# Optimization experiments

Hardware: AMD Instinct MI355X
Metric: run time of the kernel (lower is better)

## Reference

```python
import jax, jax.numpy as jnp
import numpy as np

NEG_INF = -1e30  # stands in for float('-inf') masked_fill; safe under softmax
MAX_ITERS = 6


def setup_inputs() -> dict:
    key = jax.random.key(0)
    ks = jax.random.split(key, 8)
    B, T, D, Dp, E = 8, 1500, 1536, 1024, 192
    s = lambda fan_in: 1.0 / np.sqrt(fan_in)
    return {
        "h": jax.random.normal(ks[0], (B, T, D), jnp.float32),
        "W1": jax.random.normal(ks[1], (3 * D, Dp), jnp.float32) * s(3 * D),
        "Wc": jax.random.normal(ks[2], (D, Dp), jnp.float32) * s(D),
        "W2": jax.random.normal(ks[3], (Dp, D), jnp.float32) * s(Dp),
        "b2": jnp.zeros((D,), jnp.float32),
        "w0": jax.random.normal(ks[4], (2 * D, E), jnp.float32) * s(2 * D),
        "b0": jnp.zeros((E,), jnp.float32),
        "Wstop": jax.random.normal(ks[5], (2 * D, 1), jnp.float32) * s(2 * D),
        "bstop": jnp.zeros((1,), jnp.float32),
        "threshold": jnp.full((1,), 0.5, jnp.float32),
        "C0": jnp.zeros((D,), jnp.float32),
    }


def _weighted_stats(h, a):
    # h: [B,T,D], a broadcastable to [B,T,D]
    mu = jnp.sum(a * h, axis=1)                         # [B,D]
    second = jnp.sum(a * h * h, axis=1)                 # [B,D]
    sigma = jnp.sqrt(jnp.clip(second - mu * mu, 1e-8))
    return mu, sigma


def reference(h, W1, Wc, W2, b2, w0, b0, Wstop, bstop, threshold, C0):
    B, T, D = h.shape
    th = threshold[0]

    # a_init = 1/T is constant across iterations -> hoist uniform stats and W1(e)
    mu0, sigma0 = _weighted_stats(h, jnp.float32(1.0 / T))          # [B,D]
    e = jnp.concatenate(
        [h,
         jnp.broadcast_to(mu0[:, None, :], (B, T, D)),
         jnp.broadcast_to(sigma0[:, None, :], (B, T, D))], axis=-1)  # [B,T,3D]
    base = jnp.einsum('btk,kp->btp', e, W1)                          # [B,T,Dp]

    energy_mask = jnp.mean(h * h, axis=-1) > 1e-4                    # [B,T]

    C = jnp.broadcast_to(C0[None, :], (B, D))
    stop = jnp.zeros((B,), bool)
    mask = jnp.ones((B, MAX_ITERS), bool)
    iters = jnp.arange(MAX_ITERS)

    embs, probs = [], []
    for i in range(MAX_ITERS):
        out1 = base + (C @ Wc)[:, None, :]                           # [B,T,Dp]
        out2 = jax.nn.relu(out1) @ W2 + b2                           # [B,T,D]
        att_raw = jnp.mean(out2, axis=-1)                            # [B,T]
        att_raw = jnp.where(energy_mask, att_raw, NEG_INF)
        A = jax.nn.softmax(att_raw, axis=-1)
        A = A / (jnp.sum(A, axis=1, keepdims=True) + 1e-8)

        # NOTE: faithful to source -- second weighted_stats uses out2 ('a'), not A
        mu_p, sigma_p = _weighted_stats(h, out2)                     # [B,D]
        emb = jnp.concatenate([mu_p, sigma_p], axis=-1) @ w0 + b0    # [B,E]
        emb = emb / jnp.maximum(
            jnp.linalg.norm(emb, axis=-1, keepdims=True), 1e-12)

        active = (~stop).astype(h.dtype)[:, None]
        C = C + active * (jnp.einsum('bt,btd->bd', A, h) / T)

        z = jnp.concatenate([jnp.sum(A[:, :, None] * out2, axis=1), C], axis=-1)
        p = jax.nn.sigmoid(z @ Wstop + bstop)[:, 0]                  # [B]

        newly = p < th
        mask = mask & ~(newly[:, None] & (iters[None, :] >= i))
        stop = stop | newly
        embs.append(emb)
        probs.append(p)

    E = jnp.stack(embs, axis=1)                                      # [B,6,E]
    E = E * mask[:, :, None].astype(E.dtype)
    P = jnp.stack(probs, axis=1)                                     # [B,6]
    return E, P
```

## Files before the change

### kernel.cpp

```cpp
#include <hip/hip_runtime.h>
#include <math.h>

#define NB 8
#define NT 1500
#define ND 1536
#define NP 1024
#define NE 192
#define NITER 6
#define NEGINF -1e30f

typedef __attribute__((ext_vector_type(8))) short bf16x8;
typedef __attribute__((ext_vector_type(4))) float f32x4;
typedef __attribute__((ext_vector_type(8))) unsigned short us16x8;

__device__ __forceinline__ unsigned short bf_rne(float x) {
    unsigned u = __float_as_uint(x);
    return (unsigned short)((u + 0x7FFFu + ((u >> 16) & 1u)) >> 16);
}
__device__ __forceinline__ float bf_f(unsigned short u) {
    return __uint_as_float(((unsigned)u) << 16);
}

__device__ __forceinline__ float block_reduce_sum(float v, float* red) {
    int tid = threadIdx.x;
    red[tid] = v; __syncthreads();
    for (int s = blockDim.x >> 1; s > 0; s >>= 1) {
        if (tid < s) red[tid] += red[tid + s];
        __syncthreads();
    }
    float r = red[0]; __syncthreads();
    return r;
}

__global__ void k_colstats(const float* __restrict__ h, float* __restrict__ sum1,
                           float* __restrict__ sum2) {
    int d = blockIdx.x * 256 + threadIdx.x;
    int b = blockIdx.y;
    int t0 = blockIdx.z * 125, t1 = t0 + 125;
    const float* hp = h + (size_t)b * NT * ND + d;
    float s = 0.f, s2 = 0.f;
    for (int t = t0; t < t1; ++t) { float v = hp[(size_t)t * ND]; s += v; s2 += v * v; }
    atomicAdd(&sum1[b * ND + d], s);
    atomicAdd(&sum2[b * ND + d], s2);
}

__global__ void k_stats_fin(float* __restrict__ mu0, float* __restrict__ sig0) {
    int i = blockIdx.x * 256 + threadIdx.x;
    float mu = mu0[i] * (1.f / NT);
    float sec = sig0[i] * (1.f / NT);
    mu0[i] = mu;
    sig0[i] = sqrtf(fmaxf(sec - mu * mu, 1e-8f));
}

__global__ void k_energy(const float* __restrict__ h, float* __restrict__ emask) {
    __shared__ float red[256];
    int t = blockIdx.x, b = blockIdx.y;
    const float* hp = h + ((size_t)b * NT + t) * ND;
    float s = 0.f;
    for (int d = threadIdx.x; d < ND; d += 256) { float v = hp[d]; s += v * v; }
    s = block_reduce_sum(s, red);
    if (threadIdx.x == 0) emask[b * NT + t] = (s * (1.f / ND) > 1e-4f) ? 1.f : 0.f;
}

__global__ void k_w2r(const float* __restrict__ W2, const float* __restrict__ b2,
                      float* __restrict__ w2r, float* __restrict__ b2m) {
    __shared__ float red[256];
    int p = blockIdx.x;
    float s = 0.f;
    if (p < NP) {
        const float* row = W2 + (size_t)p * ND;
        for (int d = threadIdx.x; d < ND; d += 256) s += row[d];
        s = block_reduce_sum(s, red);
        if (threadIdx.x == 0) w2r[p] = s * (1.f / ND);
    } else {
        for (int d = threadIdx.x; d < ND; d += 256) s += b2[d];
        s = block_reduce_sum(s, red);
        if (threadIdx.x == 0) b2m[0] = s * (1.f / ND);
    }
}

__global__ void k_biasb(const float* __restrict__ W1, const float* __restrict__ mu0,
                        const float* __restrict__ sig0, float* __restrict__ biasb) {
    int p = blockIdx.x * 256 + threadIdx.x;
    int d0 = blockIdx.y * 192, d1 = d0 + 192;
    float acc[NB];
#pragma unroll
    for (int b = 0; b < NB; ++b) acc[b] = 0.f;
    for (int d = d0; d < d1; ++d) {
        float wa = W1[(size_t)(ND + d) * NP + p];
        float wb = W1[(size_t)(2 * ND + d) * NP + p];
#pragma unroll
        for (int b = 0; b < NB; ++b)
            acc[b] += mu0[b * ND + d] * wa + sig0[b * ND + d] * wb;
    }
#pragma unroll
    for (int b = 0; b < NB; ++b) atomicAdd(&biasb[b * NP + p], acc[b]);
}

__global__ void k_init(float* __restrict__ C, const float* __restrict__ C0,
                       float* __restrict__ stopf) {
    int d = blockIdx.x * 256 + threadIdx.x;
    int b = blockIdx.y;
    C[b * ND + d] = C0[d];
    if (blockIdx.x == 0 && threadIdx.x == 0) stopf[b] = 0.f;
}

__global__ void k_split_w(const float* __restrict__ W, int ldw, int kcnt,
                          unsigned short* __restrict__ th, unsigned short* __restrict__ tl) {
    __shared__ float t[128][33];
    int nt = blockIdx.x, kc = blockIdx.y, tid = threadIdx.x;
    int col = tid & 127, kh = tid >> 7;
    const float* wp = W + (size_t)(kc * 32 + kh) * ldw + nt * 128 + col;
#pragma unroll
    for (int i = 0; i < 16; ++i)
        t[col][kh + 2 * i] = wp[(size_t)(2 * i) * ldw];
    __syncthreads();
    int r = tid >> 1;
    int swz = (r >> 1) & 3;
    size_t tb = ((size_t)nt * kcnt + kc) * 4096;
#pragma unroll
    for (int j = 0; j < 2; ++j) {
        int so = (tid & 1) * 2 + j;
        int s = so ^ swz;
        us16x8 hv, lv;
#pragma unroll
        for (int q = 0; q < 8; ++q) {
            float x = t[r][s * 8 + q];
            unsigned short hh = bf_rne(x);
            hv[q] = hh;
            lv[q] = bf_rne(x - bf_f(hh));
        }
        *(us16x8*)&th[tb + r * 32 + so * 8] = hv;
        *(us16x8*)&tl[tb + r * 32 + so * 8] = lv;
    }
}

__global__ void k_relu_att(const float* __restrict__ base, const float* __restrict__ cvec,
                           const float* __restrict__ w2r, unsigned short* __restrict__ th,
                           float* __restrict__ att) {
    int tr = blockIdx.x, kc = blockIdx.y, b = blockIdx.z;
    int tid = threadIdx.x;
    int r = tid >> 1, quad = tid & 1;
    int row = tr * 128 + r;
    bool ok = row < NT;
    size_t tb = ((size_t)(b * 12 + tr) * 32 + kc) * 4096;
    const float* bp = base + ((size_t)b * NT + row) * NP + kc * 32 + quad * 16;
    const float* cv = cvec + b * NP + kc * 32 + quad * 16;
    const float* wr = w2r + kc * 32 + quad * 16;
    int swz = (r >> 1) & 3;
    float asum = 0.f;
#pragma unroll
    for (int half = 0; half < 2; ++half) {
        us16x8 hv;
#pragma unroll
        for (int j = 0; j < 2; ++j) {
            float x0 = 0.f, x1 = 0.f, x2 = 0.f, x3 = 0.f;
            if (ok) {
                float4 v = *(const float4*)(bp + half * 8 + j * 4);
                float4 c4 = *(const float4*)(cv + half * 8 + j * 4);
                float4 w4 = *(const float4*)(wr + half * 8 + j * 4);
                x0 = fmaxf(v.x + c4.x, 0.f); x1 = fmaxf(v.y + c4.y, 0.f);
                x2 = fmaxf(v.z + c4.z, 0.f); x3 = fmaxf(v.w + c4.w, 0.f);
                asum += x0 * w4.x + x1 * w4.y + x2 * w4.z + x3 * w4.w;
            }
            hv[j * 4 + 0] = bf_rne(x0); hv[j * 4 + 1] = bf_rne(x1);
            hv[j * 4 + 2] = bf_rne(x2); hv[j * 4 + 3] = bf_rne(x3);
        }
        int off = r * 32 + (((quad * 2 + half) ^ swz) << 3);
        *(us16x8*)&th[tb + off] = hv;
    }
    asum += __shfl_xor(asum, 1);
    if (ok && quad == 0) atomicAdd(&att[b * NT + row], asum);
}

__global__ __launch_bounds__(256, 4) void k_gemm_relu(
    const float* __restrict__ hsrc, const unsigned short* __restrict__ at_h,
    const unsigned short* __restrict__ bt_h, const float* __restrict__ b2,
    const float* __restrict__ Aw, float* __restrict__ mup, float* __restrict__ s2p,
    float* __restrict__ zab, float* __restrict__ ahb) {
    constexpr int KC = NP / 32;
    __shared__ unsigned short As[2][4096];
    __shared__ unsigned short Bs[2][4096];
    int flat = blockIdx.x + 12 * (blockIdx.y + 12 * blockIdx.z);
    int swzf = (flat & 7) * 144 + (flat >> 3);
    int tr = swzf % 12, nt = (swzf / 12) % 12, b = swzf / 144;
    int tid = threadIdx.x;
    int lane = tid & 63, w = tid >> 6;
    int wr = w >> 1, wc = w & 1;
    int l15 = lane & 15, kg = lane >> 4;
    int sw = (l15 >> 1) & 3;
    f32x4 acc[4][4];
#pragma unroll
    for (int m = 0; m < 4; ++m)
#pragma unroll
        for (int n = 0; n < 4; ++n) acc[m][n] = (f32x4){0.f, 0.f, 0.f, 0.f};
    int aoff[4], boff[4];
#pragma unroll
    for (int m = 0; m < 4; ++m) aoff[m] = (wr * 64 + m * 16 + l15) * 32 + ((kg ^ sw) << 3);
#pragma unroll
    for (int n = 0; n < 4; ++n) boff[n] = (wc * 64 + n * 16 + l15) * 32 + ((kg ^ sw) << 3);

    const unsigned short* ga = at_h + ((size_t)(b * 12 + tr) * KC) * 4096 + lane * 8;
    const unsigned short* gb = bt_h + ((size_t)nt * KC) * 4096 + lane * 8;

    auto stage = [&](int buf, int kc) {
#pragma unroll
        for (int c = 0; c < 4; ++c) {
            int seg = w * 4 + c;
            int part = seg & 7;
            const unsigned short* src = ((seg >> 3) == 0 ? ga : gb) + (size_t)kc * 4096 + part * 512;
            unsigned short* dst = ((seg >> 3) == 0 ? &As[buf][0] : &Bs[buf][0]) + part * 512;
            __builtin_amdgcn_global_load_lds(src, dst, 16, 0, 0);
        }
    };

    stage(0, 0);
    __syncthreads();
    int cur = 0;
    for (int kc = 0; kc < KC; ++kc) {
        if (kc + 1 < KC) stage(cur ^ 1, kc + 1);
        bf16x8 af[4], bf[4];
#pragma unroll
        for (int m = 0; m < 4; ++m) af[m] = *(const bf16x8*)&As[cur][aoff[m]];
#pragma unroll
        for (int n = 0; n < 4; ++n) bf[n] = *(const bf16x8*)&Bs[cur][boff[n]];
#pragma unroll
        for (int n = 0; n < 4; ++n)
#pragma unroll
            for (int m = 0; m < 4; ++m)
                acc[m][n] = __builtin_amdgcn_mfma_f32_16x16x32_bf16(af[m], bf[n], acc[m][n], 0, 0, 0);
        __syncthreads();
        cur ^= 1;
    }

    int rowb = tr * 128 + wr * 64 + (kg << 2);
    int colb = nt * 128 + wc * 64 + l15;
    float b2c[4];
#pragma unroll
    for (int n = 0; n < 4; ++n) b2c[n] = b2[colb + n * 16];
    float pm[4] = {0, 0, 0, 0}, ps2[4] = {0, 0, 0, 0}, pza[4] = {0, 0, 0, 0}, pah[4] = {0, 0, 0, 0};
#pragma unroll
    for (int m = 0; m < 4; ++m) {
#pragma unroll
        for (int q = 0; q < 4; ++q) {
            int row = rowb + m * 16 + q;
            bool ok = row < NT;
            int rowc = ok ? row : (NT - 1);
            float okf = ok ? 1.f : 0.f;
            float a = Aw[b * NT + rowc] * okf;
            const float* hrow = hsrc + ((size_t)b * NT + rowc) * ND;
#pragma unroll
            for (int n = 0; n < 4; ++n) {
                float hv = hrow[colb + n * 16] * okf;
                float o2 = acc[m][n][q] + b2c[n];
                pm[n] = fmaf(o2, hv, pm[n]);
                ps2[n] = fmaf(o2 * hv, hv, ps2[n]);
                pza[n] = fmaf(a, o2, pza[n]);
                pah[n] = fmaf(a, hv, pah[n]);
            }
        }
    }
#pragma unroll
    for (int n = 0; n < 4; ++n) {
        pm[n] += __shfl_xor(pm[n], 16); pm[n] += __shfl_xor(pm[n], 32);
        ps2[n] += __shfl_xor(ps2[n], 16); ps2[n] += __shfl_xor(ps2[n], 32);
        pza[n] += __shfl_xor(pza[n], 16); pza[n] += __shfl_xor(pza[n], 32);
        pah[n] += __shfl_xor(pah[n], 16); pah[n] += __shfl_xor(pah[n], 32);
        if (kg == 0) {
            int col = colb + n * 16;
            atomicAdd(&mup[b * ND + col], pm[n]);
            atomicAdd(&s2p[b * ND + col], ps2[n]);
            atomicAdd(&zab[b * ND + col], pza[n]);
            atomicAdd(&ahb[b * ND + col], pah[n]);
        }
    }
}

__global__ __launch_bounds__(256, 4) void k_gemm_base(
    const float* __restrict__ hsrc, const unsigned short* __restrict__ bt_h,
    const unsigned short* __restrict__ bt_l, const float* __restrict__ biasb,
    float* __restrict__ Out) {
    constexpr int KC = ND / 32;
    __shared__ unsigned short As[4096];
    __shared__ unsigned short Bh_s[4096];
    __shared__ unsigned short Bl_s[4096];
    int flat = blockIdx.x + 12 * (blockIdx.y + 8 * blockIdx.z);
    int swzf = (flat & 7) * 96 + (flat >> 3);
    int tr = swzf % 12, nt = (swzf / 12) % 8, b = swzf / 96;
    int tid = threadIdx.x;
    int lane = tid & 63, w = tid >> 6;
    int wr = w >> 1, wc = w & 1;
    int l15 = lane & 15, kg = lane >> 4;
    int sw = (l15 >> 1) & 3;
    f32x4 acc[4][4];
#pragma unroll
    for (int m = 0; m < 4; ++m)
#pragma unroll
        for (int n = 0; n < 4; ++n) acc[m][n] = (f32x4){0.f, 0.f, 0.f, 0.f};
    int aoff[4], boff[4];
#pragma unroll
    for (int m = 0; m < 4; ++m) aoff[m] = (wr * 64 + m * 16 + l15) * 32 + ((kg ^ sw) << 3);
#pragma unroll
    for (int n = 0; n < 4; ++n) boff[n] = (wc * 64 + n * 16 + l15) * 32 + ((kg ^ sw) << 3);

    const unsigned short* gbh = bt_h + ((size_t)nt * KC) * 4096 + lane * 8;
    const unsigned short* gbl = bt_l + ((size_t)nt * KC) * 4096 + lane * 8;

    int r2 = tid >> 1, quad = tid & 1;
    int arow = tr * 128 + r2;
    bool aok = arow < NT;
    int aswz = (r2 >> 1) & 3;
    const float* hp = hsrc + ((size_t)b * NT + arow) * ND + quad * 16;

    for (int kc = 0; kc < KC; ++kc) {
#pragma unroll
        for (int c = 0; c < 4; ++c) {
            int seg = w * 4 + c;
            int part = seg & 7;
            const unsigned short* src =
                ((seg >> 3) == 0 ? gbh : gbl) + (size_t)kc * 4096 + part * 512;
            unsigned short* dst = ((seg >> 3) == 0 ? &Bh_s[0] : &Bl_s[0]) + part * 512;
            __builtin_amdgcn_global_load_lds(src, dst, 16, 0, 0);
        }
#pragma unroll
        for (int i = 0; i < 4; ++i) {
            int kk = quad * 16 + i * 4;
            float x0 = 0.f, x1 = 0.f, x2 = 0.f, x3 = 0.f;
            if (aok) {
                float4 v = *(const float4*)(hp + kc * 32 + i * 4);
                x0 = v.x; x1 = v.y; x2 = v.z; x3 = v.w;
            }
            int off = r2 * 32 + (((kk >> 3) ^ aswz) << 3) + (kk & 7);
            *(ushort4*)&As[off] = make_ushort4(bf_rne(x0), bf_rne(x1), bf_rne(x2), bf_rne(x3));
        }
        __syncthreads();
        bf16x8 af[4];
#pragma unroll
        for (int m = 0; m < 4; ++m) af[m] = *(const bf16x8*)&As[aoff[m]];
#pragma unroll
        for (int n = 0; n < 4; ++n) {
            bf16x8 bh = *(const bf16x8*)&Bh_s[boff[n]];
            bf16x8 bl = *(const bf16x8*)&Bl_s[boff[n]];
#pragma unroll
            for (int m = 0; m < 4; ++m) {
                acc[m][n] = __builtin_amdgcn_mfma_f32_16x16x32_bf16(af[m], bh, acc[m][n], 0, 0, 0);
                acc[m][n] = __builtin_amdgcn_mfma_f32_16x16x32_bf16(af[m], bl, acc[m][n], 0, 0, 0);
            }
        }
        __syncthreads();
    }

    int rowb = tr * 128 + wr * 64 + (kg << 2);
    int colb = nt * 128 + wc * 64 + l15;
#pragma unroll
    for (int m = 0; m < 4; ++m)
#pragma unroll
        for (int q = 0; q < 4; ++q) {
            int row = rowb + m * 16 + q;
            if (row < NT) {
                float* orow = Out + ((size_t)b * NT + row) * NP;
#pragma unroll
                for (int n = 0; n < 4; ++n)
                    orow[colb + n * 16] = acc[m][n][q] + biasb[b * NP + colb + n * 16];
            }
        }
}

__global__ void k_cvec(const float* __restrict__ C, const float* __restrict__ Wc,
                       float* __restrict__ cvec) {
    int p = blockIdx.x * 256 + threadIdx.x;
    int d0 = blockIdx.y * 48, d1 = d0 + 48;
    float acc[NB];
#pragma unroll
    for (int b = 0; b < NB; ++b) acc[b] = 0.f;
    for (int d = d0; d < d1; ++d) {
        float wc = Wc[(size_t)d * NP + p];
#pragma unroll
        for (int b = 0; b < NB; ++b) acc[b] += C[b * ND + d] * wc;
    }
#pragma unroll
    for (int b = 0; b < NB; ++b) atomicAdd(&cvec[b * NP + p], acc[b]);
}

__global__ void k_softmax(const float* __restrict__ att, const float* __restrict__ emask,
                          const float* __restrict__ b2m, float* __restrict__ A) {
    __shared__ float red[256];
    int b = blockIdx.x, tid = threadIdx.x;
    float bm = b2m[0];
    const float* x = att + (size_t)b * NT;
    const float* em = emask + (size_t)b * NT;
    float* a = A + (size_t)b * NT;
    float mx = -3.4e38f;
    for (int t = tid; t < NT; t += 256) {
        float v = (em[t] > 0.5f) ? x[t] + bm : NEGINF;
        mx = fmaxf(mx, v);
    }
    red[tid] = mx; __syncthreads();
    for (int s = 128; s > 0; s >>= 1) {
        if (tid < s) red[tid] = fmaxf(red[tid], red[tid + s]);
        __syncthreads();
    }
    mx = red[0]; __syncthreads();
    float sm = 0.f;
    for (int t = tid; t < NT; t += 256) {
        float v = (em[t] > 0.5f) ? x[t] + bm : NEGINF;
        float e = expf(v - mx); a[t] = e; sm += e;
    }
    float s1 = block_reduce_sum(sm, red);
    float inv1 = 1.f / s1;
    float sm2 = 0.f;
    for (int t = tid; t < NT; t += 256) { float v = a[t] * inv1; a[t] = v; sm2 += v; }
    float s2 = block_reduce_sum(sm2, red);
    float inv2 = 1.f / (s2 + 1e-8f);
    for (int t = tid; t < NT; t += 256) a[t] *= inv2;
}

__global__ void k_embacc(const float* __restrict__ red4, const float* __restrict__ w0,
                         float* __restrict__ embt) {
    __shared__ float mus[NB][48], sgs[NB][48];
    int e = threadIdx.x;
    int d0 = blockIdx.x * 48;
    const float* mup = red4;
    const float* s2p = red4 + (size_t)NB * ND;
    for (int idx = e; idx < NB * 48; idx += 192) {
        int b = idx / 48, dd = idx % 48;
        float mu = mup[b * ND + d0 + dd];
        mus[b][dd] = mu;
        sgs[b][dd] = sqrtf(fmaxf(s2p[b * ND + d0 + dd] - mu * mu, 1e-8f));
    }
    __syncthreads();
    float acc[NB];
#pragma unroll
    for (int b = 0; b < NB; ++b) acc[b] = 0.f;
    for (int dd = 0; dd < 48; ++dd) {
        float wa = w0[(size_t)(d0 + dd) * NE + e];
        float wb = w0[(size_t)(ND + d0 + dd) * NE + e];
#pragma unroll
        for (int b = 0; b < NB; ++b)
            acc[b] += mus[b][dd] * wa + sgs[b][dd] * wb;
    }
#pragma unroll
    for (int b = 0; b < NB; ++b) atomicAdd(&embt[b * NE + e], acc[b]);
}

__global__ void k_tail2(const float* __restrict__ red4, const float* __restrict__ embt,
                        const float* __restrict__ b0, const float* __restrict__ Wstop,
                        const float* __restrict__ bstop, const float* __restrict__ thr,
                        float* __restrict__ Cb, float* __restrict__ stopf,
                        float* __restrict__ Eout, float* __restrict__ Pout, int iter) {
    __shared__ float red[256];
    __shared__ float liveflag;
    int b = blockIdx.x, tid = threadIdx.x;
    const float* Ahb = red4 + (size_t)2 * NB * ND + b * ND;
    const float* zAb = red4 + (size_t)3 * NB * ND + b * ND;
    float active = (stopf[b] > 0.5f) ? 0.f : 1.f;
    float dsum = 0.f;
    for (int d = tid; d < ND; d += 256) {
        float Cn = Cb[b * ND + d] + active * (Ahb[d] * (1.f / NT));
        Cb[b * ND + d] = Cn;
        dsum += zAb[d] * Wstop[d] + Cn * Wstop[ND + d];
    }
    float s = block_reduce_sum(dsum, red);
    if (tid == 0) {
        float logit = s + bstop[0];
        float p = 1.f / (1.f + expf(-logit));
        Pout[b * NITER + iter] = p;
        bool newly = p < thr[0];
        if (newly) stopf[b] = 1.f;
        liveflag = (active > 0.5f && !newly) ? 1.f : 0.f;
    }
    __syncthreads();
    float live = liveflag;
    float emb = (tid < NE) ? (embt[b * NE + tid] + b0[tid]) : 0.f;
    float nrm = block_reduce_sum(emb * emb, red);
    float sc = live / fmaxf(sqrtf(nrm), 1e-12f);
    if (tid < NE) Eout[((size_t)b * NITER + iter) * NE + tid] = emb * sc;
}

extern "C" void kernel_launch(void* const* d_in, const int* in_sizes, int n_in,
                              void* d_out, int out_size, void* d_ws, size_t ws_size,
                              hipStream_t stream) {
    const float* h = (const float*)d_in[0];
    const float* W1 = (const float*)d_in[1];
    const float* Wc = (const float*)d_in[2];
    const float* W2 = (const float*)d_in[3];
    const float* b2 = (const float*)d_in[4];
    const float* w0 = (const float*)d_in[5];
    const float* b0 = (const float*)d_in[6];
    const float* Wstop = (const float*)d_in[7];
    const float* bstop = (const float*)d_in[8];
    const float* thr = (const float*)d_in[9];
    const float* C0 = (const float*)d_in[10];

    float* Eout = (float*)d_out;
    float* Pout = Eout + (size_t)NB * NITER * NE;

    char* wsb = (char*)d_ws;
    size_t off = 0;
    auto alloc = [&](size_t bytes) -> void* {
        void* p = wsb + off; off += (bytes + 15) & ~(size_t)15; return p;
    };

    float* base = (float*)alloc((size_t)NB * NT * NP * 4);
    unsigned short* rel_h = (unsigned short*)alloc((size_t)NB * 12 * 32 * 4096 * 2);
    unsigned short* w1t_h = (unsigned short*)alloc((size_t)8 * 48 * 4096 * 2);
    unsigned short* w1t_l = (unsigned short*)alloc((size_t)8 * 48 * 4096 * 2);
    unsigned short* w2t_h = (unsigned short*)alloc((size_t)12 * 32 * 4096 * 2);
    unsigned short* w2t_l = (unsigned short*)alloc((size_t)12 * 32 * 4096 * 2);
    float* mu0 = (float*)alloc((size_t)2 * NB * ND * 4);
    float* sig0 = mu0 + NB * ND;
    float* emask = (float*)alloc(NB * NT * 4);
    float* biasb = (float*)alloc(NB * NP * 4);
    float* w2r = (float*)alloc(NP * 4);
    float* b2m = (float*)alloc(16);
    size_t zelems = (size_t)NB * NP + NB * NT + 4 * NB * ND + NB * NE;
    float* cvec = (float*)alloc(zelems * 4);
    float* att = cvec + NB * NP;
    float* red4 = att + NB * NT;
    float* mup = red4;
    float* s2p = red4 + NB * ND;
    float* zAb = red4 + 3 * NB * ND;
    float* Ahb = red4 + 2 * NB * ND;
    float* embt = red4 + 4 * NB * ND;
    float* Abuf = (float*)alloc(NB * NT * 4);
    float* Cb = (float*)alloc(NB * ND * 4);
    float* stopf = (float*)alloc(32);
    size_t zero_bytes = zelems * 4;

    hipMemsetAsync(mu0, 0, (size_t)2 * NB * ND * 4, stream);
    hipMemsetAsync(biasb, 0, (size_t)NB * NP * 4, stream);
    k_colstats<<<dim3(ND / 256, NB, 12), 256, 0, stream>>>(h, mu0, sig0);
    k_stats_fin<<<dim3(NB * ND / 256), 256, 0, stream>>>(mu0, sig0);
    k_energy<<<dim3(NT, NB), 256, 0, stream>>>(h, emask);
    k_w2r<<<dim3(NP + 1), 256, 0, stream>>>(W2, b2, w2r, b2m);
    k_biasb<<<dim3(NP / 256, 8), 256, 0, stream>>>(W1, mu0, sig0, biasb);
    k_split_w<<<dim3(8, 48), 256, 0, stream>>>(W1, NP, 48, w1t_h, w1t_l);
    k_split_w<<<dim3(12, 32), 256, 0, stream>>>(W2, ND, 32, w2t_h, w2t_l);
    k_gemm_base<<<dim3(12, 8, NB), 256, 0, stream>>>(h, w1t_h, w1t_l, biasb, base);
    k_init<<<dim3(ND / 256, NB), 256, 0, stream>>>(Cb, C0, stopf);

    for (int i = 0; i < NITER; ++i) {
        hipMemsetAsync(cvec, 0, zero_bytes, stream);
        k_cvec<<<dim3(4, 32), 256, 0, stream>>>(Cb, Wc, cvec);
        k_relu_att<<<dim3(12, 32, NB), 256, 0, stream>>>(base, cvec, w2r, rel_h, att);
        k_softmax<<<dim3(NB), 256, 0, stream>>>(att, emask, b2m, Abuf);
        k_gemm_relu<<<dim3(12, 12, NB), 256, 0, stream>>>(
            h, rel_h, w2t_h, b2, Abuf, mup, s2p, zAb, Ahb);
        k_embacc<<<dim3(32), 192, 0, stream>>>(red4, w0, embt);
        k_tail2<<<dim3(NB), 256, 0, stream>>>(red4, embt, b0, Wstop, bstop, thr,
                                              Cb, stopf, Eout, Pout, i);
    }
}
```

Baseline: 1.086 ms.

## Pre-split h to bf16 tiles, store base in bf16, fuse energy computation

Adds a kernel that converts h once into swizzled bf16 tiles and accumulates per-row energy, replacing the separate energy kernel. The base GEMM and the per-iteration GEMM epilogue now read bf16 h tiles instead of fp32 h. The base activations are stored as bf16, halving per-iteration reads in relu_att. Both GEMMs stage 64-wide K chunks in one buffer instead of double-buffered 32-wide chunks. The aim is less memory traffic; the cost is lower precision in base and in the h used for the weighted stats, plus less load/compute overlap in the GEMM loops.

After: 1.120 ms. 3.1% more time.

```diff
diff --git a/kernel.cpp b/kernel.cpp
--- a/kernel.cpp
+++ b/kernel.cpp
@@ -50,16 +50,6 @@
     float sec = sig0[i] * (1.f / NT);
     mu0[i] = mu;
     sig0[i] = sqrtf(fmaxf(sec - mu * mu, 1e-8f));
-}
-
-__global__ void k_energy(const float* __restrict__ h, float* __restrict__ emask) {
-    __shared__ float red[256];
-    int t = blockIdx.x, b = blockIdx.y;
-    const float* hp = h + ((size_t)b * NT + t) * ND;
-    float s = 0.f;
-    for (int d = threadIdx.x; d < ND; d += 256) { float v = hp[d]; s += v * v; }
-    s = block_reduce_sum(s, red);
-    if (threadIdx.x == 0) emask[b * NT + t] = (s * (1.f / ND) > 1e-4f) ? 1.f : 0.f;
 }
 
 __global__ void k_w2r(const float* __restrict__ W2, const float* __restrict__ b2,
@@ -135,34 +125,66 @@
     }
 }
 
-__global__ void k_relu_att(const float* __restrict__ base, const float* __restrict__ cvec,
-                           const float* __restrict__ w2r, unsigned short* __restrict__ th,
-                           float* __restrict__ att) {
+__global__ void k_split_h(const float* __restrict__ h, unsigned short* __restrict__ th,
+                          float* __restrict__ energy) {
+    int tr = blockIdx.x, kc = blockIdx.y, b = blockIdx.z;
+    int tid = threadIdx.x;
+    int r = tid >> 1, quad = tid & 1;
+    int row = tr * 128 + r;
+    bool ok = row < NT;
+    size_t tb = ((size_t)(b * 12 + tr) * 48 + kc) * 4096;
+    const float* hp = h + ((size_t)b * NT + (ok ? row : 0)) * ND + kc * 32 + quad * 16;
+    int swz = (r >> 1) & 3;
+    float es = 0.f;
+#pragma unroll
+    for (int half = 0; half < 2; ++half) {
+        us16x8 hv;
+#pragma unroll
+        for (int j = 0; j < 2; ++j) {
+            float x0 = 0.f, x1 = 0.f, x2 = 0.f, x3 = 0.f;
+            if (ok) {
+                float4 v = *(const float4*)(hp + half * 8 + j * 4);
+                x0 = v.x; x1 = v.y; x2 = v.z; x3 = v.w;
+                es += x0 * x0 + x1 * x1 + x2 * x2 + x3 * x3;
+            }
+            hv[j * 4 + 0] = bf_rne(x0); hv[j * 4 + 1] = bf_rne(x1);
+            hv[j * 4 + 2] = bf_rne(x2); hv[j * 4 + 3] = bf_rne(x3);
+        }
+        int off = r * 32 + (((quad * 2 + half) ^ swz) << 3);
+        *(us16x8*)&th[tb + off] = hv;
+    }
+    es += __shfl_xor(es, 1);
+    if (ok && quad == 0) atomicAdd(&energy[b * NT + row], es);
+}
+
+__global__ void k_relu_att(const unsigned short* __restrict__ base16,
+                           const float* __restrict__ cvec, const float* __restrict__ w2r,
+                           unsigned short* __restrict__ th, float* __restrict__ att) {
     int tr = blockIdx.x, kc = blockIdx.y, b = blockIdx.z;
     int tid = threadIdx.x;
     int r = tid >> 1, quad = tid & 1;
     int row = tr * 128 + r;
     bool ok = row < NT;
     size_t tb = ((size_t)(b * 12 + tr) * 32 + kc) * 4096;
-    const float* bp = base + ((size_t)b * NT + row) * NP + kc * 32 + quad * 16;
+    const unsigned short* bp = base16 + ((size_t)b * NT + (ok ? row : 0)) * NP + kc * 32 + quad * 16;
     const float* cv = cvec + b * NP + kc * 32 + quad * 16;
     const float* wr = w2r + kc * 32 + quad * 16;
     int swz = (r >> 1) & 3;
     float asum = 0.f;
 #pragma unroll
     for (int half = 0; half < 2; ++half) {
+        us16x8 bv = (us16x8){0, 0, 0, 0, 0, 0, 0, 0};
+        if (ok) bv = *(const us16x8*)(bp + half * 8);
         us16x8 hv;
 #pragma unroll
         for (int j = 0; j < 2; ++j) {
-            float x0 = 0.f, x1 = 0.f, x2 = 0.f, x3 = 0.f;
-            if (ok) {
-                float4 v = *(const float4*)(bp + half * 8 + j * 4);
-                float4 c4 = *(const float4*)(cv + half * 8 + j * 4);
-                float4 w4 = *(const float4*)(wr + half * 8 + j * 4);
-                x0 = fmaxf(v.x + c4.x, 0.f); x1 = fmaxf(v.y + c4.y, 0.f);
-                x2 = fmaxf(v.z + c4.z, 0.f); x3 = fmaxf(v.w + c4.w, 0.f);
-                asum += x0 * w4.x + x1 * w4.y + x2 * w4.z + x3 * w4.w;
-            }
+            float4 c4 = *(const float4*)(cv + half * 8 + j * 4);
+            float4 w4 = *(const float4*)(wr + half * 8 + j * 4);
+            float x0 = fmaxf(bf_f(bv[j * 4 + 0]) + c4.x, 0.f);
+            float x1 = fmaxf(bf_f(bv[j * 4 + 1]) + c4.y, 0.f);
+            float x2 = fmaxf(bf_f(bv[j * 4 + 2]) + c4.z, 0.f);
+            float x3 = fmaxf(bf_f(bv[j * 4 + 3]) + c4.w, 0.f);
+            if (ok) asum += x0 * w4.x + x1 * w4.y + x2 * w4.z + x3 * w4.w;
             hv[j * 4 + 0] = bf_rne(x0); hv[j * 4 + 1] = bf_rne(x1);
             hv[j * 4 + 2] = bf_rne(x2); hv[j * 4 + 3] = bf_rne(x3);
         }
@@ -174,13 +196,13 @@
 }
 
 __global__ __launch_bounds__(256, 4) void k_gemm_relu(
-    const float* __restrict__ hsrc, const unsigned short* __restrict__ at_h,
+    const unsigned short* __restrict__ ht, const unsigned short* __restrict__ at_h,
     const unsigned short* __restrict__ bt_h, const float* __restrict__ b2,
     const float* __restrict__ Aw, float* __restrict__ mup, float* __restrict__ s2p,
     float* __restrict__ zab, float* __restrict__ ahb) {
-    constexpr int KC = NP / 32;
-    __shared__ unsigned short As[2][4096];
-    __shared__ unsigned short Bs[2][4096];
+    constexpr int KC2 = NP / 64;
+    __shared__ __align__(16) unsigned short As[8192];
+    __shared__ __align__(16) unsigned short Bs[8192];
     int flat = blockIdx.x + 12 * (blockIdx.y + 12 * blockIdx.z);
     int swzf = (flat & 7) * 144 + (flat >> 3);
     int tr = swzf % 12, nt = (swzf / 12) % 12, b = swzf / 144;
@@ -200,41 +222,39 @@
 #pragma unroll
     for (int n = 0; n < 4; ++n) boff[n] = (wc * 64 + n * 16 + l15) * 32 + ((kg ^ sw) << 3);
 
-    const unsigned short* ga = at_h + ((size_t)(b * 12 + tr) * KC) * 4096 + lane * 8;
-    const unsigned short* gb = bt_h + ((size_t)nt * KC) * 4096 + lane * 8;
-
-    auto stage = [&](int buf, int kc) {
-#pragma unroll
-        for (int c = 0; c < 4; ++c) {
-            int seg = w * 4 + c;
-            int part = seg & 7;
-            const unsigned short* src = ((seg >> 3) == 0 ? ga : gb) + (size_t)kc * 4096 + part * 512;
-            unsigned short* dst = ((seg >> 3) == 0 ? &As[buf][0] : &Bs[buf][0]) + part * 512;
+    const unsigned short* ga = at_h + ((size_t)(b * 12 + tr) * 32) * 4096 + lane * 8;
+    const unsigned short* gb = bt_h + ((size_t)nt * 32) * 4096 + lane * 8;
+
+    for (int kc2 = 0; kc2 < KC2; ++kc2) {
+#pragma unroll
+        for (int c = 0; c < 8; ++c) {
+            int seg = w * 8 + c;
+            int part = seg & 15, mat = seg >> 4;
+            const unsigned short* src = (mat ? gb : ga) + (size_t)kc2 * 8192 + part * 512;
+            unsigned short* dst = (mat ? &Bs[0] : &As[0]) + part * 512;
             __builtin_amdgcn_global_load_lds(src, dst, 16, 0, 0);
         }
-    };
-
-    stage(0, 0);
-    __syncthreads();
-    int cur = 0;
-    for (int kc = 0; kc < KC; ++kc) {
-        if (kc + 1 < KC) stage(cur ^ 1, kc + 1);
-        bf16x8 af[4], bf[4];
-#pragma unroll
-        for (int m = 0; m < 4; ++m) af[m] = *(const bf16x8*)&As[cur][aoff[m]];
-#pragma unroll
-        for (int n = 0; n < 4; ++n) bf[n] = *(const bf16x8*)&Bs[cur][boff[n]];
-#pragma unroll
-        for (int n = 0; n < 4; ++n)
-#pragma unroll
-            for (int m = 0; m < 4; ++m)
-                acc[m][n] = __builtin_amdgcn_mfma_f32_16x16x32_bf16(af[m], bf[n], acc[m][n], 0, 0, 0);
         __syncthreads();
-        cur ^= 1;
+#pragma unroll
+        for (int half = 0; half < 2; ++half) {
+            int ho = half * 4096;
+            bf16x8 af[4], bfr[4];
+#pragma unroll
+            for (int m = 0; m < 4; ++m) af[m] = *(const bf16x8*)&As[ho + aoff[m]];
+#pragma unroll
+            for (int n = 0; n < 4; ++n) bfr[n] = *(const bf16x8*)&Bs[ho + boff[n]];
+#pragma unroll
+            for (int n = 0; n < 4; ++n)
+#pragma unroll
+                for (int m = 0; m < 4; ++m)
+                    acc[m][n] = __builtin_amdgcn_mfma_f32_16x16x32_bf16(af[m], bfr[n], acc[m][n], 0, 0, 0);
+        }
+        __syncthreads();
     }
 
     int rowb = tr * 128 + wr * 64 + (kg << 2);
     int colb = nt * 128 + wc * 64 + l15;
+    const unsigned short* htb = ht + (size_t)(b * 12 + tr) * 48 * 4096;
     float b2c[4];
 #pragma unroll
     for (int n = 0; n < 4; ++n) b2c[n] = b2[colb + n * 16];
@@ -244,14 +264,16 @@
 #pragma unroll
         for (int q = 0; q < 4; ++q) {
             int row = rowb + m * 16 + q;
+            int r_in = wr * 64 + (kg << 2) + m * 16 + q;
             bool ok = row < NT;
-            int rowc = ok ? row : (NT - 1);
             float okf = ok ? 1.f : 0.f;
-            float a = Aw[b * NT + rowc] * okf;
-            const float* hrow = hsrc + ((size_t)b * NT + rowc) * ND;
+            float a = Aw[b * NT + (ok ? row : (NT - 1))] * okf;
+            int rsw = (r_in >> 1) & 3;
 #pragma unroll
             for (int n = 0; n < 4; ++n) {
-                float hv = hrow[colb + n * 16] * okf;
+                int col = colb + n * 16;
+                float hv = bf_f(htb[(size_t)(col >> 5) * 4096 + r_in * 32 +
+                                    ((((col & 31) >> 3) ^ rsw) << 3) + (col & 7)]) * okf;
                 float o2 = acc[m][n][q] + b2c[n];
                 pm[n] = fmaf(o2, hv, pm[n]);
                 ps2[n] = fmaf(o2 * hv, hv, ps2[n]);
@@ -276,14 +298,14 @@
     }
 }
 
-__global__ __launch_bounds__(256, 4) void k_gemm_base(
-    const float* __restrict__ hsrc, const unsigned short* __restrict__ bt_h,
+__global__ __launch_bounds__(256, 3) void k_gemm_base(
+    const unsigned short* __restrict__ ht, const unsigned short* __restrict__ bt_h,
     const unsigned short* __restrict__ bt_l, const float* __restrict__ biasb,
-    float* __restrict__ Out) {
-    constexpr int KC = ND / 32;
-    __shared__ unsigned short As[4096];
-    __shared__ unsigned short Bh_s[4096];
-    __shared__ unsigned short Bl_s[4096];
+    unsigned short* __restrict__ Out16) {
+    constexpr int KC2 = ND / 64;
+    __shared__ __align__(16) unsigned short As[8192];
+    __shared__ __align__(16) unsigned short Bh_s[8192];
+    __shared__ __align__(16) unsigned short Bl_s[8192];
     int flat = blockIdx.x + 12 * (blockIdx.y + 8 * blockIdx.z);
     int swzf = (flat & 7) * 96 + (flat >> 3);
     int tr = swzf % 12, nt = (swzf / 12) % 8, b = swzf / 96;
@@ -303,48 +325,37 @@
 #pragma unroll
     for (int n = 0; n < 4; ++n) boff[n] = (wc * 64 + n * 16 + l15) * 32 + ((kg ^ sw) << 3);
 
-    const unsigned short* gbh = bt_h + ((size_t)nt * KC) * 4096 + lane * 8;
-    const unsigned short* gbl = bt_l + ((size_t)nt * KC) * 4096 + lane * 8;
-
-    int r2 = tid >> 1, quad = tid & 1;
-    int arow = tr * 128 + r2;
-    bool aok = arow < NT;
-    int aswz = (r2 >> 1) & 3;
-    const float* hp = hsrc + ((size_t)b * NT + arow) * ND + quad * 16;
-
-    for (int kc = 0; kc < KC; ++kc) {
-#pragma unroll
-        for (int c = 0; c < 4; ++c) {
-            int seg = w * 4 + c;
-            int part = seg & 7;
+    const unsigned short* ga = ht + ((size_t)(b * 12 + tr) * 48) * 4096 + lane * 8;
+    const unsigned short* gbh = bt_h + ((size_t)nt * 48) * 4096 + lane * 8;
+    const unsigned short* gbl = bt_l + ((size_t)nt * 48) * 4096 + lane * 8;
+
+    for (int kc2 = 0; kc2 < KC2; ++kc2) {
+#pragma unroll
+        for (int c = 0; c < 12; ++c) {
+            int seg = w * 12 + c;
+            int part = seg & 15, mat = seg >> 4;
             const unsigned short* src =
-                ((seg >> 3) == 0 ? gbh : gbl) + (size_t)kc * 4096 + part * 512;
-            unsigned short* dst = ((seg >> 3) == 0 ? &Bh_s[0] : &Bl_s[0]) + part * 512;
+                (mat == 0 ? ga : mat == 1 ? gbh : gbl) + (size_t)kc2 * 8192 + part * 512;
+            unsigned short* dst =
+                (mat == 0 ? &As[0] : mat == 1 ? &Bh_s[0] : &Bl_s[0]) + part * 512;
             __builtin_amdgcn_global_load_lds(src, dst, 16, 0, 0);
         }
-#pragma unroll
-        for (int i = 0; i < 4; ++i) {
-            int kk = quad * 16 + i * 4;
-            float x0 = 0.f, x1 = 0.f, x2 = 0.f, x3 = 0.f;
-            if (aok) {
-                float4 v = *(const float4*)(hp + kc * 32 + i * 4);
-                x0 = v.x; x1 = v.y; x2 = v.z; x3 = v.w;
-            }
-            int off = r2 * 32 + (((kk >> 3) ^ aswz) << 3) + (kk & 7);
-            *(ushort4*)&As[off] = make_ushort4(bf_rne(x0), bf_rne(x1), bf_rne(x2), bf_rne(x3));
-        }
         __syncthreads();
-        bf16x8 af[4];
-#pragma unroll
-        for (int m = 0; m < 4; ++m) af[m] = *(const bf16x8*)&As[aoff[m]];
-#pragma unroll
-        for (int n = 0; n < 4; ++n) {
-            bf16x8 bh = *(const bf16x8*)&Bh_s[boff[n]];
-            bf16x8 bl = *(const bf16x8*)&Bl_s[boff[n]];
-#pragma unroll
-            for (int m = 0; m < 4; ++m) {
-                acc[m][n] = __builtin_amdgcn_mfma_f32_16x16x32_bf16(af[m], bh, acc[m][n], 0, 0, 0);
-                acc[m][n] = __builtin_amdgcn_mfma_f32_16x16x32_bf16(af[m], bl, acc[m][n], 0, 0, 0);
+#pragma unroll
+        for (int half = 0; half < 2; ++half) {
+            int ho = half * 4096;
+            bf16x8 af[4];
+#pragma unroll
+            for (int m = 0; m < 4; ++m) af[m] = *(const bf16x8*)&As[ho + aoff[m]];
+#pragma unroll
+            for (int n = 0; n < 4; ++n) {
+                bf16x8 bh = *(const bf16x8*)&Bh_s[ho + boff[n]];
+                bf16x8 bl = *(const bf16x8*)&Bl_s[ho + boff[n]];
+#pragma unroll
+                for (int m = 0; m < 4; ++m) {
+                    acc[m][n] = __builtin_amdgcn_mfma_f32_16x16x32_bf16(af[m], bh, acc[m][n], 0, 0, 0);
+                    acc[m][n] = __builtin_amdgcn_mfma_f32_16x16x32_bf16(af[m], bl, acc[m][n], 0, 0, 0);
+                }
             }
         }
         __syncthreads();
@@ -358,10 +369,11 @@
         for (int q = 0; q < 4; ++q) {
             int row = rowb + m * 16 + q;
             if (row < NT) {
-                float* orow = Out + ((size_t)b * NT + row) * NP;
+                unsigned short* orow = Out16 + ((size_t)b * NT + row) * NP;
 #pragma unroll
                 for (int n = 0; n < 4; ++n)
-                    orow[colb + n * 16] = acc[m][n][q] + biasb[b * NP + colb + n * 16];
+                    orow[colb + n * 16] =
+                        bf_rne(acc[m][n][q] + biasb[b * NP + colb + n * 16]);
             }
         }
 }
@@ -382,17 +394,17 @@
     for (int b = 0; b < NB; ++b) atomicAdd(&cvec[b * NP + p], acc[b]);
 }
 
-__global__ void k_softmax(const float* __restrict__ att, const float* __restrict__ emask,
+__global__ void k_softmax(const float* __restrict__ att, const float* __restrict__ energy,
                           const float* __restrict__ b2m, float* __restrict__ A) {
     __shared__ float red[256];
     int b = blockIdx.x, tid = threadIdx.x;
     float bm = b2m[0];
     const float* x = att + (size_t)b * NT;
-    const float* em = emask + (size_t)b * NT;
+    const float* en = energy + (size_t)b * NT;
     float* a = A + (size_t)b * NT;
     float mx = -3.4e38f;
     for (int t = tid; t < NT; t += 256) {
-        float v = (em[t] > 0.5f) ? x[t] + bm : NEGINF;
+        float v = (en[t] * (1.f / ND) > 1e-4f) ? x[t] + bm : NEGINF;
         mx = fmaxf(mx, v);
     }
     red[tid] = mx; __syncthreads();
@@ -403,7 +415,7 @@
     mx = red[0]; __syncthreads();
     float sm = 0.f;
     for (int t = tid; t < NT; t += 256) {
-        float v = (em[t] > 0.5f) ? x[t] + bm : NEGINF;
+        float v = (en[t] * (1.f / ND) > 1e-4f) ? x[t] + bm : NEGINF;
         float e = expf(v - mx); a[t] = e; sm += e;
     }
     float s1 = block_reduce_sum(sm, red);
@@ -501,16 +513,18 @@
         void* p = wsb + off; off += (bytes + 15) & ~(size_t)15; return p;
     };
 
-    float* base = (float*)alloc((size_t)NB * NT * NP * 4);
+    unsigned short* base16 = (unsigned short*)alloc((size_t)NB * NT * NP * 2);
     unsigned short* rel_h = (unsigned short*)alloc((size_t)NB * 12 * 32 * 4096 * 2);
+    unsigned short* ht_h = (unsigned short*)alloc((size_t)NB * 12 * 48 * 4096 * 2);
     unsigned short* w1t_h = (unsigned short*)alloc((size_t)8 * 48 * 4096 * 2);
     unsigned short* w1t_l = (unsigned short*)alloc((size_t)8 * 48 * 4096 * 2);
     unsigned short* w2t_h = (unsigned short*)alloc((size_t)12 * 32 * 4096 * 2);
     unsigned short* w2t_l = (unsigned short*)alloc((size_t)12 * 32 * 4096 * 2);
-    float* mu0 = (float*)alloc((size_t)2 * NB * ND * 4);
+    size_t pz = (size_t)2 * NB * ND + NB * NT + NB * NP;
+    float* mu0 = (float*)alloc(pz * 4);
     float* sig0 = mu0 + NB * ND;
-    float* emask = (float*)alloc(NB * NT * 4);
-    float* biasb = (float*)alloc(NB * NP * 4);
+    float* energy = sig0 + NB * ND;
+    float* biasb = energy + NB * NT;
     float* w2r = (float*)alloc(NP * 4);
     float* b2m = (float*)alloc(16);
     size_t zelems = (size_t)NB * NP + NB * NT + 4 * NB * ND + NB * NE;
@@ -519,33 +533,32 @@
     float* red4 = att + NB * NT;
     float* mup = red4;
     float* s2p = red4 + NB * ND;
+    float* Ahb = red4 + 2 * NB * ND;
     float* zAb = red4 + 3 * NB * ND;
-    float* Ahb = red4 + 2 * NB * ND;
     float* embt = red4 + 4 * NB * ND;
     float* Abuf = (float*)alloc(NB * NT * 4);
     float* Cb = (float*)alloc(NB * ND * 4);
     float* stopf = (float*)alloc(32);
     size_t zero_bytes = zelems * 4;
 
-    hipMemsetAsync(mu0, 0, (size_t)2 * NB * ND * 4, stream);
-    hipMemsetAsync(biasb, 0, (size_t)NB * NP * 4, stream);
+    hipMemsetAsync(mu0, 0, pz * 4, stream);
     k_colstats<<<dim3(ND / 256, NB, 12), 256, 0, stream>>>(h, mu0, sig0);
     k_stats_fin<<<dim3(NB * ND / 256), 256, 0, stream>>>(mu0, sig0);
-    k_energy<<<dim3(NT, NB), 256, 0, stream>>>(h, emask);
     k_w2r<<<dim3(NP + 1), 256, 0, stream>>>(W2, b2, w2r, b2m);
     k_biasb<<<dim3(NP / 256, 8), 256, 0, stream>>>(W1, mu0, sig0, biasb);
     k_split_w<<<dim3(8, 48), 256, 0, stream>>>(W1, NP, 48, w1t_h, w1t_l);
     k_split_w<<<dim3(12, 32), 256, 0, stream>>>(W2, ND, 32, w2t_h, w2t_l);
-    k_gemm_base<<<dim3(12, 8, NB), 256, 0, stream>>>(h, w1t_h, w1t_l, biasb, base);
+    k_split_h<<<dim3(12, 48, NB), 256, 0, stream>>>(h, ht_h, energy);
+    k_gemm_base<<<dim3(12, 8, NB), 256, 0, stream>>>(ht_h, w1t_h, w1t_l, biasb, base16);
     k_init<<<dim3(ND / 256, NB), 256, 0, stream>>>(Cb, C0, stopf);
 
     for (int i = 0; i < NITER; ++i) {
         hipMemsetAsync(cvec, 0, zero_bytes, stream);
         k_cvec<<<dim3(4, 32), 256, 0, stream>>>(Cb, Wc, cvec);
-        k_relu_att<<<dim3(12, 32, NB), 256, 0, stream>>>(base, cvec, w2r, rel_h, att);
-        k_softmax<<<dim3(NB), 256, 0, stream>>>(att, emask, b2m, Abuf);
+        k_relu_att<<<dim3(12, 32, NB), 256, 0, stream>>>(base16, cvec, w2r, rel_h, att);
+        k_softmax<<<dim3(NB), 256, 0, stream>>>(att, energy, b2m, Abuf);
         k_gemm_relu<<<dim3(12, 12, NB), 256, 0, stream>>>(
-            h, rel_h, w2t_h, b2, Abuf, mup, s2p, zAb, Ahb);
+            ht_h, rel_h, w2t_h, b2, Abuf, mup, s2p, zAb, Ahb);
         k_embacc<<<dim3(32), 192, 0, stream>>>(red4, w0, embt);
         k_tail2<<<dim3(NB), 256, 0, stream>>>(red4, embt, b0, Wstop, bstop, thr,
                                               Cb, stopf, Eout, Pout, i);
```
